# Performance work log

Measured on AMD Instinct MI355X. Metric: run time of the kernel, lower is better.

The kernel has to match this reference:

```python
import jax, jax.numpy as jnp
import numpy as np

B, T, I, R, O = 1, 2048, 8, 4096, 8
SPECTRAL_RADIUS = 0.9
SPARSITY = 0.1


def setup_inputs() -> dict:
    key = jax.random.key(0)
    k1, k2, k3, k4, k5, k6 = jax.random.split(key, 6)
    x = jax.random.normal(k1, (B, T, I), dtype=jnp.float32)
    Win = jax.random.normal(k2, (R, I), dtype=jnp.float32)
    W = jax.random.normal(k3, (R, R), dtype=jnp.float32)
    # sparse mask + spectral-radius scaling (circular-law approx: rho(sparse gaussian) ~ sqrt(sparsity*R))
    mask = (jax.random.uniform(k4, (R, R)) < SPARSITY).astype(jnp.float32)
    W = W * mask * (SPECTRAL_RADIUS / jnp.sqrt(SPARSITY * R))
    Wout_w = jax.random.normal(k5, (O, R), dtype=jnp.float32) / jnp.sqrt(R)
    Wout_b = jax.random.normal(k6, (O,), dtype=jnp.float32) * 0.01
    return {"x": x, "Win": Win, "W": W, "Wout_w": Wout_w, "Wout_b": Wout_b}


def reference(x, Win, W, Wout_w, Wout_b):
    Bb = x.shape[0]
    h0 = jnp.zeros((Bb, W.shape[0]), dtype=x.dtype)

    def step(h, xt):  # xt: [B, I]
        h = jnp.tanh(xt @ Win.T + h @ W.T)          # [B, R]
        out = h @ Wout_w.T + Wout_b                  # [B, O]
        return h, out

    xs = jnp.swapaxes(x, 0, 1)                       # [T, B, I]
    _, outs = jax.lax.scan(step, h0, xs)             # outs: [T, B, O]
    return jnp.swapaxes(outs, 0, 1)                  # [B, T, O]
```

## Files before the change

kernel.cpp:

```cpp
#include <hip/hip_runtime.h>
#include <math.h>


#define T_STEPS 2048
#define R_DIM   4096
#define I_DIM   8
#define O_DIM   8
#define NWG     128
#define ROWS_PER_WG (R_DIM / NWG)
#define POOL_CAP 16384
#define BLOCK    512

typedef float v4f __attribute__((ext_vector_type(4)));

__device__ float        g_hist[(size_t)T_STEPS * R_DIM];
__device__ unsigned int g_flag[NWG * 32];

__global__ void esn_init_kernel() {
    for (int i = threadIdx.x; i < NWG * 32; i += blockDim.x)
        __hip_atomic_store(&g_flag[i], 0u, __ATOMIC_RELAXED,
                           __HIP_MEMORY_SCOPE_SYSTEM);
}

__launch_bounds__(BLOCK, 1)
__global__ void esn_recur_kernel(const float* __restrict__ x,
                                 const float* __restrict__ Win,
                                 const float* __restrict__ W) {
    __shared__ uint2 s_pool[POOL_CAP];
    __shared__ float s_h[R_DIM];
    __shared__ int   s_start[ROWS_PER_WG + 1];
    __shared__ int   s_cnt[ROWS_PER_WG];
    __shared__ float s_win[ROWS_PER_WG][I_DIM];

    const int wg   = blockIdx.x;
    const int tid  = threadIdx.x;
    const int lane = tid & 63;
    const int wave = tid >> 6;
    const int row0 = wg * ROWS_PER_WG;

    for (int rr = wave; rr < ROWS_PER_WG; rr += 8) {
        const float* wrow = W + (size_t)(row0 + rr) * R_DIM;
        int cnt = 0;
        for (int base = 0; base < R_DIM; base += 64) {
            float v = wrow[base + lane];
            cnt += __popcll(__ballot(v != 0.0f));
        }
        if (lane == 0) s_cnt[rr] = cnt;
    }
    __syncthreads();
    if (tid == 0) {
        int acc = 0;
        for (int rr = 0; rr < ROWS_PER_WG; ++rr) {
            s_start[rr] = (acc < POOL_CAP) ? acc : POOL_CAP;
            acc += s_cnt[rr];
        }
        s_start[ROWS_PER_WG] = (acc < POOL_CAP) ? acc : POOL_CAP;
    }
    __syncthreads();
    for (int rr = wave; rr < ROWS_PER_WG; rr += 8) {
        const float* wrow = W + (size_t)(row0 + rr) * R_DIM;
        int off = s_start[rr];
        for (int base = 0; base < R_DIM; base += 64) {
            float v = wrow[base + lane];
            unsigned long long m = __ballot(v != 0.0f);
            int pre = __popcll(m & ((1ull << lane) - 1ull));
            if (v != 0.0f) {
                int pos = off + pre;
                if (pos < POOL_CAP) {
                    s_pool[pos].x = __float_as_uint(v);
                    s_pool[pos].y = base + lane;
                }
            }
            off += __popcll(m);
        }
    }
    if (tid < ROWS_PER_WG * I_DIM) {
        int rr = tid / I_DIM, c = tid % I_DIM;
        s_win[rr][c] = Win[(size_t)(row0 + rr) * I_DIM + c];
    }
    __syncthreads();

    const int row16 = tid >> 4;
    const int sub   = tid & 15;
    const int start = s_start[row16];
    const int cnt   = s_start[row16 + 1] - start;

    const int  src_wg  = (wave << 4) + (lane & 15);
    const bool poller  = (lane < 16);
    const unsigned* fp = &g_flag[src_wg << 5];

    for (int t = 0; t < T_STEPS; ++t) {
        const float4* xp = (const float4*)(x + (size_t)t * I_DIM);
        const float4 xa = xp[0];
        const float4 xb = xp[1];

        if (t > 0) {
            const unsigned ut = (unsigned)t;
            for (;;) {
                unsigned v = poller
                    ? __hip_atomic_load(fp, __ATOMIC_RELAXED,
                                        __HIP_MEMORY_SCOPE_SYSTEM)
                    : ut;
                if (__all(v >= ut)) break;
                __builtin_amdgcn_s_sleep(1);
            }
            const v4f* bp = (const v4f*)(g_hist + (size_t)(t - 1) * R_DIM
                                         + (size_t)tid * 8);
            v4f r0, r1;
            asm volatile(
                "global_load_dwordx4 %0, %2, off sc0 sc1\n\t"
                "global_load_dwordx4 %1, %2, off offset:16 sc0 sc1\n\t"
                "s_waitcnt vmcnt(0)"
                : "=v"(r0), "=v"(r1)
                : "v"(bp)
                : "memory");
            v4f* dst = (v4f*)(s_h + (size_t)tid * 8);
            dst[0] = r0;
            dst[1] = r1;
            __syncthreads();
        }

        float acc = 0.0f;
        if (t > 0) {
            for (int e = start + sub; e < start + cnt; e += 16) {
                uint2 p = s_pool[e];
                acc += __uint_as_float(p.x) * s_h[p.y];
            }
        }
        acc += __shfl_xor(acc, 8, 16);
        acc += __shfl_xor(acc, 4, 16);
        acc += __shfl_xor(acc, 2, 16);
        acc += __shfl_xor(acc, 1, 16);

        if (sub == 0) {
            float a = acc;
            a += s_win[row16][0] * xa.x;
            a += s_win[row16][1] * xa.y;
            a += s_win[row16][2] * xa.z;
            a += s_win[row16][3] * xa.w;
            a += s_win[row16][4] * xb.x;
            a += s_win[row16][5] * xb.y;
            a += s_win[row16][6] * xb.z;
            a += s_win[row16][7] * xb.w;
            float h = tanhf(a);
            __hip_atomic_store(&g_hist[(size_t)t * R_DIM + row0 + row16], h,
                               __ATOMIC_RELAXED, __HIP_MEMORY_SCOPE_SYSTEM);
        }
        asm volatile("s_waitcnt vmcnt(0)" ::: "memory");
        __syncthreads();
        if (tid == 0)
            __hip_atomic_store(&g_flag[wg << 5], (unsigned)(t + 1),
                               __ATOMIC_RELAXED, __HIP_MEMORY_SCOPE_SYSTEM);
    }
}

__global__ void esn_out_kernel(const float* __restrict__ Wout_w,
                               const float* __restrict__ Wout_b,
                               float* __restrict__ out) {
    const int t = blockIdx.x;
    const int lane = threadIdx.x;
    const float* hp = g_hist + (size_t)t * R_DIM;
    float acc[O_DIM];
    #pragma unroll
    for (int o = 0; o < O_DIM; ++o) acc[o] = 0.0f;
    for (int i = lane; i < R_DIM; i += 256) {
        float h0 = __hip_atomic_load(hp + i,       __ATOMIC_RELAXED, __HIP_MEMORY_SCOPE_SYSTEM);
        float h1 = __hip_atomic_load(hp + i + 64,  __ATOMIC_RELAXED, __HIP_MEMORY_SCOPE_SYSTEM);
        float h2 = __hip_atomic_load(hp + i + 128, __ATOMIC_RELAXED, __HIP_MEMORY_SCOPE_SYSTEM);
        float h3 = __hip_atomic_load(hp + i + 192, __ATOMIC_RELAXED, __HIP_MEMORY_SCOPE_SYSTEM);
        #pragma unroll
        for (int o = 0; o < O_DIM; ++o) acc[o] += h0 * Wout_w[(size_t)o * R_DIM + i];
        #pragma unroll
        for (int o = 0; o < O_DIM; ++o) acc[o] += h1 * Wout_w[(size_t)o * R_DIM + i + 64];
        #pragma unroll
        for (int o = 0; o < O_DIM; ++o) acc[o] += h2 * Wout_w[(size_t)o * R_DIM + i + 128];
        #pragma unroll
        for (int o = 0; o < O_DIM; ++o) acc[o] += h3 * Wout_w[(size_t)o * R_DIM + i + 192];
    }
    #pragma unroll
    for (int o = 0; o < O_DIM; ++o) {
        float a = acc[o];
        a += __shfl_xor(a, 32);
        a += __shfl_xor(a, 16);
        a += __shfl_xor(a, 8);
        a += __shfl_xor(a, 4);
        a += __shfl_xor(a, 2);
        a += __shfl_xor(a, 1);
        if (lane == 0) out[(size_t)t * O_DIM + o] = a + Wout_b[o];
    }
}

extern "C" void kernel_launch(void* const* d_in, const int* in_sizes, int n_in,
                              void* d_out, int out_size, void* d_ws, size_t ws_size,
                              hipStream_t stream) {
    const float* x    = (const float*)d_in[0];
    const float* Win  = (const float*)d_in[1];
    const float* W    = (const float*)d_in[2];
    const float* Ww   = (const float*)d_in[3];
    const float* Wb   = (const float*)d_in[4];
    float* out = (float*)d_out;

    hipLaunchKernelGGL(esn_init_kernel, dim3(1), dim3(256), 0, stream);

    void* args[] = { (void*)&x, (void*)&Win, (void*)&W };
    hipLaunchCooperativeKernel((void*)esn_recur_kernel, dim3(NWG), dim3(BLOCK),
                               args, 0, stream);

    hipLaunchKernelGGL(esn_out_kernel, dim3(T_STEPS), dim3(64), 0, stream,
                       Ww, Wb, out);
}
```

Before: 8.600 ms.

## Cache sparse recurrent weights in registers and halve workgroup count

The recurrence now uses 64 workgroups of 1024 threads instead of 128 of 512, so each step has half as many flags to poll and the cross-workgroup barrier is cheaper. The compressed nonzeros of each row are loaded once, in two LDS passes, into per-thread registers: 36 values and 16-bit packed byte offsets. Each step then avoids reading the weight pool from LDS and runs a fixed, fully unrolled loop. The cost is higher register pressure and wasted iterations on zero padding. Any row with more than 576 nonzeros would be silently truncated.

```diff
diff --git a/kernel.cpp b/kernel.cpp
--- a/kernel.cpp
+++ b/kernel.cpp
@@ -6,10 +6,12 @@
 #define R_DIM   4096
 #define I_DIM   8
 #define O_DIM   8
-#define NWG     128
+#define NWG     64
 #define ROWS_PER_WG (R_DIM / NWG)
+#define HALF_ROWS 32
 #define POOL_CAP 16384
-#define BLOCK    512
+#define BLOCK    1024
+#define NS       36
 
 typedef float v4f __attribute__((ext_vector_type(4)));
 
@@ -28,8 +30,8 @@
                                  const float* __restrict__ W) {
     __shared__ uint2 s_pool[POOL_CAP];
     __shared__ float s_h[R_DIM];
-    __shared__ int   s_start[ROWS_PER_WG + 1];
-    __shared__ int   s_cnt[ROWS_PER_WG];
+    __shared__ int   s_start[HALF_ROWS + 1];
+    __shared__ int   s_cnt[HALF_ROWS];
     __shared__ float s_win[ROWS_PER_WG][I_DIM];
 
     const int wg   = blockIdx.x;
@@ -38,41 +40,67 @@
     const int wave = tid >> 6;
     const int row0 = wg * ROWS_PER_WG;
 
-    for (int rr = wave; rr < ROWS_PER_WG; rr += 8) {
-        const float* wrow = W + (size_t)(row0 + rr) * R_DIM;
-        int cnt = 0;
-        for (int base = 0; base < R_DIM; base += 64) {
-            float v = wrow[base + lane];
-            cnt += __popcll(__ballot(v != 0.0f));
-        }
-        if (lane == 0) s_cnt[rr] = cnt;
-    }
-    __syncthreads();
-    if (tid == 0) {
-        int acc = 0;
-        for (int rr = 0; rr < ROWS_PER_WG; ++rr) {
-            s_start[rr] = (acc < POOL_CAP) ? acc : POOL_CAP;
-            acc += s_cnt[rr];
-        }
-        s_start[ROWS_PER_WG] = (acc < POOL_CAP) ? acc : POOL_CAP;
-    }
-    __syncthreads();
-    for (int rr = wave; rr < ROWS_PER_WG; rr += 8) {
-        const float* wrow = W + (size_t)(row0 + rr) * R_DIM;
-        int off = s_start[rr];
-        for (int base = 0; base < R_DIM; base += 64) {
-            float v = wrow[base + lane];
-            unsigned long long m = __ballot(v != 0.0f);
-            int pre = __popcll(m & ((1ull << lane) - 1ull));
-            if (v != 0.0f) {
-                int pos = off + pre;
-                if (pos < POOL_CAP) {
-                    s_pool[pos].x = __float_as_uint(v);
-                    s_pool[pos].y = base + lane;
+    const int row16 = tid >> 4;
+    const int sub   = tid & 15;
+
+    float    rv[NS];
+    unsigned ri[NS / 2];
+
+    for (int pass = 0; pass < 2; ++pass) {
+        const int prow0 = row0 + pass * HALF_ROWS;
+        for (int rr = wave; rr < HALF_ROWS; rr += 16) {
+            const float* wrow = W + (size_t)(prow0 + rr) * R_DIM;
+            int cnt = 0;
+            for (int base = 0; base < R_DIM; base += 64) {
+                float v = wrow[base + lane];
+                cnt += __popcll(__ballot(v != 0.0f));
+            }
+            if (lane == 0) s_cnt[rr] = cnt;
+        }
+        __syncthreads();
+        if (tid == 0) {
+            int acc = 0;
+            for (int rr = 0; rr < HALF_ROWS; ++rr) {
+                s_start[rr] = (acc < POOL_CAP) ? acc : POOL_CAP;
+                acc += s_cnt[rr];
+            }
+            s_start[HALF_ROWS] = (acc < POOL_CAP) ? acc : POOL_CAP;
+        }
+        __syncthreads();
+        for (int rr = wave; rr < HALF_ROWS; rr += 16) {
+            const float* wrow = W + (size_t)(prow0 + rr) * R_DIM;
+            int off = s_start[rr];
+            for (int base = 0; base < R_DIM; base += 64) {
+                float v = wrow[base + lane];
+                unsigned long long m = __ballot(v != 0.0f);
+                int pre = __popcll(m & ((1ull << lane) - 1ull));
+                if (v != 0.0f) {
+                    int pos = off + pre;
+                    if (pos < POOL_CAP) {
+                        s_pool[pos].x = __float_as_uint(v);
+                        s_pool[pos].y = (base + lane) * 4;
+                    }
                 }
-            }
-            off += __popcll(m);
-        }
+                off += __popcll(m);
+            }
+        }
+        __syncthreads();
+        const int lr = row16 - pass * HALF_ROWS;
+        if (lr >= 0 && lr < HALF_ROWS) {
+            const int st = s_start[lr];
+            const int en = s_start[lr + 1];
+            #pragma unroll
+            for (int m = 0; m < NS; ++m) {
+                const int e = st + sub + (m << 4);
+                float    v = 0.0f;
+                unsigned b = 0u;
+                if (e < en) { uint2 p = s_pool[e]; v = __uint_as_float(p.x); b = p.y; }
+                rv[m] = v;
+                if ((m & 1) == 0) ri[m >> 1] = b;
+                else              ri[m >> 1] |= (b << 16);
+            }
+        }
+        __syncthreads();
     }
     if (tid < ROWS_PER_WG * I_DIM) {
         int rr = tid / I_DIM, c = tid % I_DIM;
@@ -80,13 +108,8 @@
     }
     __syncthreads();
 
-    const int row16 = tid >> 4;
-    const int sub   = tid & 15;
-    const int start = s_start[row16];
-    const int cnt   = s_start[row16 + 1] - start;
-
-    const int  src_wg  = (wave << 4) + (lane & 15);
-    const bool poller  = (lane < 16);
+    const int  src_wg  = (wave << 2) + (lane & 3);
+    const bool poller  = (lane < 4);
     const unsigned* fp = &g_flag[src_wg << 5];
 
     for (int t = 0; t < T_STEPS; ++t) {
@@ -105,26 +128,26 @@
                 __builtin_amdgcn_s_sleep(1);
             }
             const v4f* bp = (const v4f*)(g_hist + (size_t)(t - 1) * R_DIM
-                                         + (size_t)tid * 8);
-            v4f r0, r1;
+                                         + (size_t)tid * 4);
+            v4f r0;
             asm volatile(
-                "global_load_dwordx4 %0, %2, off sc0 sc1\n\t"
-                "global_load_dwordx4 %1, %2, off offset:16 sc0 sc1\n\t"
+                "global_load_dwordx4 %0, %1, off sc0 sc1\n\t"
                 "s_waitcnt vmcnt(0)"
-                : "=v"(r0), "=v"(r1)
+                : "=v"(r0)
                 : "v"(bp)
                 : "memory");
-            v4f* dst = (v4f*)(s_h + (size_t)tid * 8);
-            dst[0] = r0;
-            dst[1] = r1;
+            *(v4f*)(s_h + (size_t)tid * 4) = r0;
             __syncthreads();
         }
 
         float acc = 0.0f;
         if (t > 0) {
-            for (int e = start + sub; e < start + cnt; e += 16) {
-                uint2 p = s_pool[e];
-                acc += __uint_as_float(p.x) * s_h[p.y];
+            #pragma unroll
+            for (int m = 0; m < NS; ++m) {
+                const unsigned ba = (m & 1) ? (ri[m >> 1] >> 16)
+                                            : (ri[m >> 1] & 0xffffu);
+                const float hv = *(const float*)((const char*)s_h + ba);
+                acc += rv[m] * hv;
             }
         }
         acc += __shfl_xor(acc, 8, 16);
```

Measured after the change: 7.061 ms. 17.9% less time.
